# Optimization experiments

Hardware: AMD Instinct MI355X
Metric: run time of the kernel (lower is better)

The kernel has to match this reference:

```python
import jax, jax.numpy as jnp
import numpy as np

N_HEAD = 12

def setup_inputs() -> dict:
    key = jax.random.key(0)
    ks = jax.random.split(key, 5)
    B, T, C = 4, 2048, 768
    scale = 0.02
    return {
        "x": jax.random.normal(ks[0], (B, T, C), dtype=jnp.float32),
        "W_attn": jax.random.normal(ks[1], (C, 3 * C), dtype=jnp.float32) * scale,
        "b_attn": jax.random.normal(ks[2], (3 * C,), dtype=jnp.float32) * scale,
        "W_proj": jax.random.normal(ks[3], (C, C), dtype=jnp.float32) * scale,
        "b_proj": jax.random.normal(ks[4], (C,), dtype=jnp.float32) * scale,
    }

def reference(x, W_attn, b_attn, W_proj, b_proj):
    B, T, C = x.shape
    H = N_HEAD
    D = C // H  # head dim
    qkv = x @ W_attn + b_attn  # [B,T,3C]
    q, k, v = jnp.split(qkv, 3, axis=-1)
    # [B,H,T,D]
    q = q.reshape(B, T, H, D).transpose(0, 2, 1, 3)
    k = k.reshape(B, T, H, D).transpose(0, 2, 1, 3)
    v = v.reshape(B, T, H, D).transpose(0, 2, 1, 3)
    scores = jnp.einsum('bhqd,bhkd->bhqk', q, k) / jnp.sqrt(jnp.float32(D))
    causal = jnp.tril(jnp.ones((T, T), dtype=bool))
    scores = jnp.where(causal[None, None, :, :], scores, jnp.float32(-jnp.inf))
    attn = jax.nn.softmax(scores, axis=-1)
    out = jnp.einsum('bhqk,bhkd->bhqd', attn, v)  # [B,H,T,D]
    out = out.transpose(0, 2, 1, 3).reshape(B, T, C)
    return out @ W_proj + b_proj
```

## Files before the change

kernel.cpp:

```cpp
#include <hip/hip_runtime.h>

typedef float f32x4 __attribute__((ext_vector_type(4)));
typedef __bf16 bf16x8 __attribute__((ext_vector_type(8)));
typedef unsigned short u16x8 __attribute__((ext_vector_type(8)));
typedef unsigned short u16x4 __attribute__((ext_vector_type(4)));

#define MFMA16(a, b, c) __builtin_amdgcn_mfma_f32_16x16x32_bf16((a), (b), (c), 0, 0, 0)

__device__ __forceinline__ unsigned short f2bf(float f) {
    __bf16 h = (__bf16)f;
    union { __bf16 h; unsigned short u; } c; c.h = h;
    return c.u;
}

__device__ __forceinline__ void gload_lds16(const unsigned short* g, unsigned short* l) {
    __builtin_amdgcn_global_load_lds(
        (const __attribute__((address_space(1))) unsigned int*)g,
        (__attribute__((address_space(3))) unsigned int*)l, 16, 0, 0);
}

__global__ void k_convert_bf16(const float* __restrict__ in,
                               unsigned short* __restrict__ out, int n) {
    int i = (blockIdx.x * 256 + threadIdx.x) * 4;
    if (i + 3 < n) {
        float4 v = *reinterpret_cast<const float4*>(in + i);
        ushort4 o;
        o.x = f2bf(v.x); o.y = f2bf(v.y); o.z = f2bf(v.z); o.w = f2bf(v.w);
        *reinterpret_cast<ushort4*>(out + i) = o;
    }
}

__global__ void k_transpose_bf16(const float* __restrict__ in,
                                 unsigned short* __restrict__ out, int R, int C) {
    __shared__ unsigned short tile[32][33];
    int bx = blockIdx.x * 32;
    int by = blockIdx.y * 32;
    int tx = threadIdx.x;
    int ty = threadIdx.y;
    #pragma unroll
    for (int i = ty; i < 32; i += 8)
        tile[i][tx] = f2bf(in[(size_t)(by + i) * C + bx + tx]);
    __syncthreads();
    #pragma unroll
    for (int i = ty; i < 32; i += 8)
        out[(size_t)(bx + i) * R + by + tx] = tile[tx][i];
}

template<int EPI>
__global__ __launch_bounds__(512) void k_gemm_bt(
    const unsigned short* __restrict__ A,
    const unsigned short* __restrict__ Bt,
    const float* __restrict__ bias,
    unsigned short* __restrict__ Qo,
    unsigned short* __restrict__ Ko,
    unsigned short* __restrict__ Vto,
    float* __restrict__ Co,
    int K)
{
    __shared__ unsigned short SM[(256 + 128) * 64];
    unsigned short* As = SM;
    unsigned short* Bs = SM + 256 * 64;
    const int nwg = gridDim.x * gridDim.y;
    const int bid0 = blockIdx.y * gridDim.x + blockIdx.x;
    const int logical = (bid0 & 7) * (nwg >> 3) + (bid0 >> 3);
    const int bm = logical / gridDim.x;
    const int bn = logical % gridDim.x;
    const int tid = threadIdx.x;
    const int w = tid >> 6, l = tid & 63;
    const int wm = w >> 1, wn = w & 1;
    const int ln = l & 15, kb = l >> 4;

    f32x4 acc[4][4];
    #pragma unroll
    for (int i = 0; i < 4; ++i)
        #pragma unroll
        for (int j = 0; j < 4; ++j)
            #pragma unroll
            for (int r = 0; r < 4; ++r) acc[i][j][r] = 0.f;

    const unsigned short* Ab = A + (size_t)(bm * 256) * K;
    const unsigned short* Bb = Bt + (size_t)(bn * 128) * K;

    const int srow = tid >> 3;
    const int sslot = tid & 7;
    const int csw = (sslot ^ (srow & 7)) * 8;

    for (int k0 = 0; k0 < K; k0 += 64) {
        #pragma unroll
        for (int j = 0; j < 4; ++j) {
            const int r = j * 64 + srow;
            gload_lds16(&Ab[(size_t)r * K + k0 + csw], &As[r * 64 + sslot * 8]);
        }
        #pragma unroll
        for (int j = 0; j < 2; ++j) {
            const int r = j * 64 + srow;
            gload_lds16(&Bb[(size_t)r * K + k0 + csw], &Bs[r * 64 + sslot * 8]);
        }
        __syncthreads();
        #pragma unroll
        for (int kh = 0; kh < 2; ++kh) {
            bf16x8 af[4], bfr[4];
            #pragma unroll
            for (int mt = 0; mt < 4; ++mt) {
                const int row = wm * 64 + mt * 16 + ln;
                const int slot = ((kh << 2) | kb) ^ (row & 7);
                af[mt] = *reinterpret_cast<const bf16x8*>(&As[row * 64 + slot * 8]);
            }
            #pragma unroll
            for (int nt = 0; nt < 4; ++nt) {
                const int row = wn * 64 + nt * 16 + ln;
                const int slot = ((kh << 2) | kb) ^ (row & 7);
                bfr[nt] = *reinterpret_cast<const bf16x8*>(&Bs[row * 64 + slot * 8]);
            }
            #pragma unroll
            for (int mt = 0; mt < 4; ++mt)
                #pragma unroll
                for (int nt = 0; nt < 4; ++nt)
                    acc[mt][nt] = MFMA16(af[mt], bfr[nt], acc[mt][nt]);
        }
        __syncthreads();
    }

    const float SC = 0.1803368801111204f;

    if (EPI == 0 && bn >= 12) {
        unsigned short* Ts = SM;
        const int cl_w = wn * 64;
        #pragma unroll
        for (int hh2 = 0; hh2 < 2; ++hh2) {
            if ((wm >> 1) == hh2) {
                #pragma unroll
                for (int mt = 0; mt < 4; ++mt) {
                    #pragma unroll
                    for (int nt = 0; nt < 4; ++nt) {
                        const int cl = cl_w + nt * 16 + ln;
                        const float bv = bias[bn * 128 + cl];
                        #pragma unroll
                        for (int r = 0; r < 4; ++r) {
                            const int rl = (wm & 1) * 64 + mt * 16 + kb * 4 + r;
                            const int pos = cl * 128 + ((((rl >> 3) ^ (cl & 7)) << 3) | (rl & 7));
                            Ts[pos] = f2bf(acc[mt][nt][r] + bv);
                        }
                    }
                }
            }
            __syncthreads();
            {
                const int cl = tid >> 2;
                const int col = bn * 128 + cl;
                const int cc = col - 1536;
                const int hh = cc >> 6, dd = cc & 63;
                #pragma unroll
                for (int j8 = 0; j8 < 4; ++j8) {
                    const int rb = (tid & 3) * 4 + j8;
                    u16x8 val = *reinterpret_cast<const u16x8*>(&Ts[cl * 128 + ((rb ^ (cl & 7)) << 3)]);
                    const int tg = bm * 256 + hh2 * 128 + rb * 8;
                    const int bb = tg >> 11;
                    const int tloc = tg & 2047;
                    const int grp = tloc & ~31;
                    const int jj = (tloc >> 3) & 3;
                    const int tlo = grp + 8 * ((2 * jj) & 3) + 4 * (jj >> 1);
                    const int thi = grp + 8 * ((2 * jj + 1) & 3) + 4 * (jj >> 1);
                    unsigned short* basep = &Vto[((size_t)((bb * 12 + hh) * 64 + dd)) * 2048];
                    *reinterpret_cast<u16x4*>(basep + tlo) =
                        __builtin_shufflevector(val, val, 0, 1, 2, 3);
                    *reinterpret_cast<u16x4*>(basep + thi) =
                        __builtin_shufflevector(val, val, 4, 5, 6, 7);
                }
            }
            __syncthreads();
        }
        return;
    }

    #pragma unroll
    for (int mt = 0; mt < 4; ++mt) {
        #pragma unroll
        for (int nt = 0; nt < 4; ++nt) {
            const int col = bn * 128 + wn * 64 + nt * 16 + ln;
            #pragma unroll
            for (int r = 0; r < 4; ++r) {
                const int row = bm * 256 + wm * 64 + mt * 16 + kb * 4 + r;
                float v = acc[mt][nt][r] + bias[col];
                if (EPI == 0) {
                    int cc = col >= 768 ? col - 768 : col;
                    int h = cc >> 6, d = cc & 63;
                    int b = row >> 11, t = row & 2047;
                    if (col < 768)
                        Qo[((size_t)((b * 12 + h) * 2048 + t)) * 64 + d] = f2bf(v * SC);
                    else
                        Ko[((size_t)((b * 12 + h) * 2048 + t)) * 64 + d] = f2bf(v);
                } else {
                    Co[(size_t)row * 768 + col] = v;
                }
            }
        }
    }
}

__global__ __launch_bounds__(256) void k_attn(
    const unsigned short* __restrict__ Q,
    const unsigned short* __restrict__ Kk,
    const unsigned short* __restrict__ Vt,
    unsigned short* __restrict__ Oo)
{
    __shared__ unsigned short Ks[2][64 * 64];
    __shared__ unsigned short Vs[2][64 * 64];
    const int bid0 = blockIdx.x;
    const int xcd = bid0 & 7;
    const int loc = bid0 >> 3;
    const int qb = 15 - (loc / 6);
    const int bh = xcd * 6 + (loc % 6);
    const int tid = threadIdx.x;
    const int w = tid >> 6, l = tid & 63;
    const int ln = l & 15, kb = l >> 4;
    const int kbq = kb * 4;
    const int b = bh / 12, h = bh - b * 12;
    const int q0w = qb * 128 + w * 32;

    const unsigned short* Qb = Q + (size_t)bh * 2048 * 64;
    const unsigned short* Kb = Kk + (size_t)bh * 2048 * 64;
    const unsigned short* Vb = Vt + (size_t)bh * 64 * 2048;

    bf16x8 qf[2][2];
    #pragma unroll
    for (int qn = 0; qn < 2; ++qn) {
        const unsigned short* qr = &Qb[(size_t)(q0w + qn * 16 + ln) * 64 + kb * 8];
        qf[qn][0] = *reinterpret_cast<const bf16x8*>(qr);
        qf[qn][1] = *reinterpret_cast<const bf16x8*>(qr + 32);
    }

    bf16x8 vones;
    #pragma unroll
    for (int e = 0; e < 8; ++e) vones[e] = (__bf16)1.0f;
    const f32x4 fzero = {0.f, 0.f, 0.f, 0.f};

    f32x4 oaccT[2][4];
    f32x4 den[2];
    #pragma unroll
    for (int qn = 0; qn < 2; ++qn) {
        #pragma unroll
        for (int r = 0; r < 4; ++r) den[qn][r] = 0.f;
        #pragma unroll
        for (int dt = 0; dt < 4; ++dt)
            #pragma unroll
            for (int r = 0; r < 4; ++r) oaccT[qn][dt][r] = 0.f;
    }

    const int srow = tid >> 3;
    const int sslot = tid & 7;
    const int csw = (sslot ^ (srow & 7)) * 8;
    const int ntile = 2 * qb + 2;
    const int lastkt = (q0w + 31) >> 6;

    #define STAGE(kt_, buf_)                                                        \
        {                                                                           \
            const int kb_ = (kt_) * 64;                                             \
            _Pragma("unroll")                                                       \
            for (int j = 0; j < 2; ++j) {                                           \
                const int r = j * 32 + srow;                                        \
                gload_lds16(&Kb[(size_t)(kb_ + r) * 64 + csw],                      \
                            &Ks[buf_][r * 64 + sslot * 8]);                         \
                gload_lds16(&Vb[(size_t)r * 2048 + kb_ + csw],                      \
                            &Vs[buf_][r * 64 + sslot * 8]);                         \
            }                                                                       \
        }

    STAGE(0, 0);

    for (int kt = 0; kt < ntile; ++kt) {
        const int buf = kt & 1;
        asm volatile("s_waitcnt vmcnt(0)" ::: "memory");
        __builtin_amdgcn_sched_barrier(0);
        __builtin_amdgcn_s_barrier();
        if (kt + 1 < ntile) STAGE(kt + 1, buf ^ 1);

        if (kt <= lastkt) {
            const int kbase = kt * 64;
            const unsigned short* Ksb = &Ks[buf][0];
            const unsigned short* Vsb = &Vs[buf][0];
            bf16x8 kf[4][2];
            #pragma unroll
            for (int km = 0; km < 4; ++km) {
                const int row = km * 16 + ln;
                #pragma unroll
                for (int dh = 0; dh < 2; ++dh) {
                    const int slot = ((dh << 2) | kb) ^ (row & 7);
                    kf[km][dh] = *reinterpret_cast<const bf16x8*>(&Ksb[row * 64 + slot * 8]);
                }
            }
            f32x4 st[4][2];
            __builtin_amdgcn_s_setprio(1);
            #pragma unroll
            for (int km = 0; km < 4; ++km)
                #pragma unroll
                for (int qn = 0; qn < 2; ++qn) {
                    st[km][qn] = MFMA16(kf[km][0], qf[qn][0], fzero);
                    st[km][qn] = MFMA16(kf[km][1], qf[qn][1], st[km][qn]);
                }
            __builtin_amdgcn_s_setprio(0);
            bf16x8 vf[4][2];
            #pragma unroll
            for (int dt = 0; dt < 4; ++dt) {
                const int row = dt * 16 + ln;
                #pragma unroll
                for (int kh = 0; kh < 2; ++kh) {
                    const int slot = ((kh << 2) | kb) ^ (row & 7);
                    vf[dt][kh] = *reinterpret_cast<const bf16x8*>(&Vsb[row * 64 + slot * 8]);
                }
            }

            const bool diag = (kt == lastkt);
            #pragma unroll
            for (int qn = 0; qn < 2; ++qn) {
                const int qrow = q0w + qn * 16 + ln;
                #pragma unroll
                for (int km = 0; km < 4; ++km) {
                    #pragma unroll
                    for (int r = 0; r < 4; ++r) {
                        float sv = st[km][qn][r];
                        if (diag) {
                            const int key = kbase + km * 16 + kbq + r;
                            sv = (key <= qrow) ? sv : -1e30f;
                        }
                        st[km][qn][r] = __builtin_amdgcn_exp2f(sv);
                    }
                }
            }
            bf16x8 pa[2][2];
            #pragma unroll
            for (int qn = 0; qn < 2; ++qn)
                #pragma unroll
                for (int kh = 0; kh < 2; ++kh) {
                    bf16x8 t;
                    #pragma unroll
                    for (int r = 0; r < 4; ++r) {
                        t[r]     = (__bf16)st[2 * kh][qn][r];
                        t[r + 4] = (__bf16)st[2 * kh + 1][qn][r];
                    }
                    pa[qn][kh] = t;
                }
            __builtin_amdgcn_s_setprio(1);
            #pragma unroll
            for (int qn = 0; qn < 2; ++qn) {
                #pragma unroll
                for (int dt = 0; dt < 4; ++dt) {
                    oaccT[qn][dt] = MFMA16(pa[qn][0], vf[dt][0], oaccT[qn][dt]);
                    oaccT[qn][dt] = MFMA16(pa[qn][1], vf[dt][1], oaccT[qn][dt]);
                }
                den[qn] = MFMA16(pa[qn][0], vones, den[qn]);
                den[qn] = MFMA16(pa[qn][1], vones, den[qn]);
            }
            __builtin_amdgcn_s_setprio(0);
        }
    }

    #pragma unroll
    for (int qn = 0; qn < 2; ++qn) {
        #pragma unroll
        for (int r = 0; r < 4; ++r) {
            const float inv = 1.0f / den[qn][r];
            const int t = q0w + qn * 16 + kbq + r;
            #pragma unroll
            for (int dt = 0; dt < 4; ++dt)
                Oo[((size_t)(b * 2048 + t)) * 768 + h * 64 + dt * 16 + ln] =
                    f2bf(oaccT[qn][dt][r] * inv);
        }
    }
}

extern "C" void kernel_launch(void* const* d_in, const int* in_sizes, int n_in,
                              void* d_out, int out_size, void* d_ws, size_t ws_size,
                              hipStream_t stream) {
    const float* x      = (const float*)d_in[0];
    const float* W_attn = (const float*)d_in[1];
    const float* b_attn = (const float*)d_in[2];
    const float* W_proj = (const float*)d_in[3];
    const float* b_proj = (const float*)d_in[4];
    float* out = (float*)d_out;

    char* ws = (char*)d_ws;
    const size_t SZ_X  = (size_t)8192 * 768 * 2;
    const size_t SZ_WA = (size_t)2304 * 768 * 2;
    const size_t SZ_WP = (size_t)768 * 768 * 2;
    const size_t SZ_T  = (size_t)8192 * 768 * 2;

    unsigned short* x_bf = (unsigned short*)(ws);
    unsigned short* wa_t = (unsigned short*)(ws + SZ_X);
    unsigned short* wp_t = (unsigned short*)(ws + SZ_X + SZ_WA);
    unsigned short* Qb   = (unsigned short*)(ws + SZ_X + SZ_WA + SZ_WP);
    unsigned short* Kb   = (unsigned short*)(ws + SZ_X + SZ_WA + SZ_WP + SZ_T);
    unsigned short* Vtb  = (unsigned short*)(ws + SZ_X + SZ_WA + SZ_WP + 2 * SZ_T);
    unsigned short* attn_o = x_bf;

    k_convert_bf16<<<6144, 256, 0, stream>>>(x, x_bf, 8192 * 768);
    dim3 tb(32, 8);
    k_transpose_bf16<<<dim3(2304 / 32, 768 / 32), tb, 0, stream>>>(W_attn, wa_t, 768, 2304);
    k_transpose_bf16<<<dim3(768 / 32, 768 / 32), tb, 0, stream>>>(W_proj, wp_t, 768, 768);
    k_gemm_bt<0><<<dim3(18, 32), 512, 0, stream>>>(x_bf, wa_t, b_attn, Qb, Kb, Vtb, nullptr, 768);
    k_attn<<<768, 256, 0, stream>>>(Qb, Kb, Vtb, attn_o);
    k_gemm_bt<1><<<dim3(6, 32), 512, 0, stream>>>(attn_o, wp_t, b_proj, nullptr, nullptr, nullptr, out, 768);
}
```

Measured before the change: 138.8 us.

## Make attention single-wave blocks loading K/V directly into registers

```diff
diff --git a/kernel.cpp b/kernel.cpp
--- a/kernel.cpp
+++ b/kernel.cpp
@@ -198,25 +198,23 @@
     }
 }
 
-__global__ __launch_bounds__(256) void k_attn(
+__global__ __launch_bounds__(64) void k_attn(
     const unsigned short* __restrict__ Q,
     const unsigned short* __restrict__ Kk,
     const unsigned short* __restrict__ Vt,
     unsigned short* __restrict__ Oo)
 {
-    __shared__ unsigned short Ks[2][64 * 64];
-    __shared__ unsigned short Vs[2][64 * 64];
     const int bid0 = blockIdx.x;
     const int xcd = bid0 & 7;
-    const int loc = bid0 >> 3;
-    const int qb = 15 - (loc / 6);
-    const int bh = xcd * 6 + (loc % 6);
+    const int idx = bid0 >> 3;
+    const int hloc = idx % 6;
+    const int qc = 63 - idx / 6;
+    const int bh = xcd * 6 + hloc;
     const int tid = threadIdx.x;
-    const int w = tid >> 6, l = tid & 63;
-    const int ln = l & 15, kb = l >> 4;
+    const int ln = tid & 15, kb = tid >> 4;
     const int kbq = kb * 4;
     const int b = bh / 12, h = bh - b * 12;
-    const int q0w = qb * 128 + w * 32;
+    const int q0w = qc * 32;
 
     const unsigned short* Qb = Q + (size_t)bh * 2048 * 64;
     const unsigned short* Kb = Kk + (size_t)bh * 2048 * 64;
@@ -247,111 +245,91 @@
             for (int r = 0; r < 4; ++r) oaccT[qn][dt][r] = 0.f;
     }
 
-    const int srow = tid >> 3;
-    const int sslot = tid & 7;
-    const int csw = (sslot ^ (srow & 7)) * 8;
-    const int ntile = 2 * qb + 2;
-    const int lastkt = (q0w + 31) >> 6;
-
-    #define STAGE(kt_, buf_)                                                        \
-        {                                                                           \
-            const int kb_ = (kt_) * 64;                                             \
-            _Pragma("unroll")                                                       \
-            for (int j = 0; j < 2; ++j) {                                           \
-                const int r = j * 32 + srow;                                        \
-                gload_lds16(&Kb[(size_t)(kb_ + r) * 64 + csw],                      \
-                            &Ks[buf_][r * 64 + sslot * 8]);                         \
-                gload_lds16(&Vb[(size_t)r * 2048 + kb_ + csw],                      \
-                            &Vs[buf_][r * 64 + sslot * 8]);                         \
-            }                                                                       \
-        }
-
-    STAGE(0, 0);
+    const int ntile = (q0w + 31) / 64 + 1;
+    const int lastkt = ntile - 1;
+
+    bf16x8 kf[4][2], vf[4][2];
+    #pragma unroll
+    for (int km = 0; km < 4; ++km) {
+        const unsigned short* kr = &Kb[(size_t)(km * 16 + ln) * 64 + kb * 8];
+        kf[km][0] = *reinterpret_cast<const bf16x8*>(kr);
+        kf[km][1] = *reinterpret_cast<const bf16x8*>(kr + 32);
+    }
+    #pragma unroll
+    for (int dt = 0; dt < 4; ++dt) {
+        const unsigned short* vr = &Vb[(size_t)(dt * 16 + ln) * 2048 + kb * 8];
+        vf[dt][0] = *reinterpret_cast<const bf16x8*>(vr);
+        vf[dt][1] = *reinterpret_cast<const bf16x8*>(vr + 32);
+    }
 
     for (int kt = 0; kt < ntile; ++kt) {
-        const int buf = kt & 1;
-        asm volatile("s_waitcnt vmcnt(0)" ::: "memory");
-        __builtin_amdgcn_sched_barrier(0);
-        __builtin_amdgcn_s_barrier();
-        if (kt + 1 < ntile) STAGE(kt + 1, buf ^ 1);
-
-        if (kt <= lastkt) {
-            const int kbase = kt * 64;
-            const unsigned short* Ksb = &Ks[buf][0];
-            const unsigned short* Vsb = &Vs[buf][0];
-            bf16x8 kf[4][2];
+        const int kbase = kt * 64;
+        f32x4 st[4][2];
+        #pragma unroll
+        for (int km = 0; km < 4; ++km)
+            #pragma unroll
+            for (int qn = 0; qn < 2; ++qn) {
+                st[km][qn] = MFMA16(kf[km][0], qf[qn][0], fzero);
+                st[km][qn] = MFMA16(kf[km][1], qf[qn][1], st[km][qn]);
+            }
+        if (kt + 1 < ntile) {
+            const int nb = kbase + 64;
             #pragma unroll
             for (int km = 0; km < 4; ++km) {
-                const int row = km * 16 + ln;
-                #pragma unroll
-                for (int dh = 0; dh < 2; ++dh) {
-                    const int slot = ((dh << 2) | kb) ^ (row & 7);
-                    kf[km][dh] = *reinterpret_cast<const bf16x8*>(&Ksb[row * 64 + slot * 8]);
-                }
-            }
-            f32x4 st[4][2];
-            __builtin_amdgcn_s_setprio(1);
-            #pragma unroll
-            for (int km = 0; km < 4; ++km)
-                #pragma unroll
-                for (int qn = 0; qn < 2; ++qn) {
-                    st[km][qn] = MFMA16(kf[km][0], qf[qn][0], fzero);
-                    st[km][qn] = MFMA16(kf[km][1], qf[qn][1], st[km][qn]);
-                }
-            __builtin_amdgcn_s_setprio(0);
-            bf16x8 vf[4][2];
+                const unsigned short* kr = &Kb[(size_t)(nb + km * 16 + ln) * 64 + kb * 8];
+                kf[km][0] = *reinterpret_cast<const bf16x8*>(kr);
+                kf[km][1] = *reinterpret_cast<const bf16x8*>(kr + 32);
+            }
+        }
+
+        const bool diag = (kt == lastkt);
+        #pragma unroll
+        for (int qn = 0; qn < 2; ++qn) {
+            const int qrow = q0w + qn * 16 + ln;
+            #pragma unroll
+            for (int km = 0; km < 4; ++km) {
+                #pragma unroll
+                for (int r = 0; r < 4; ++r) {
+                    float sv = st[km][qn][r];
+                    if (diag) {
+                        const int key = kbase + km * 16 + kbq + r;
+                        sv = (key <= qrow) ? sv : -1e30f;
+                    }
+                    st[km][qn][r] = __builtin_amdgcn_exp2f(sv);
+                }
+            }
+        }
+        bf16x8 pa[2][2];
+        #pragma unroll
+        for (int qn = 0; qn < 2; ++qn)
+            #pragma unroll
+            for (int kh = 0; kh < 2; ++kh) {
+                bf16x8 t;
+                #pragma unroll
+                for (int r = 0; r < 4; ++r) {
+                    t[r]     = (__bf16)st[2 * kh][qn][r];
+                    t[r + 4] = (__bf16)st[2 * kh + 1][qn][r];
+                }
+                pa[qn][kh] = t;
+            }
+        #pragma unroll
+        for (int qn = 0; qn < 2; ++qn) {
             #pragma unroll
             for (int dt = 0; dt < 4; ++dt) {
-                const int row = dt * 16 + ln;
-                #pragma unroll
-                for (int kh = 0; kh < 2; ++kh) {
-                    const int slot = ((kh << 2) | kb) ^ (row & 7);
-                    vf[dt][kh] = *reinterpret_cast<const bf16x8*>(&Vsb[row * 64 + slot * 8]);
-                }
-            }
-
-            const bool diag = (kt == lastkt);
-            #pragma unroll
-            for (int qn = 0; qn < 2; ++qn) {
-                const int qrow = q0w + qn * 16 + ln;
-                #pragma unroll
-                for (int km = 0; km < 4; ++km) {
-                    #pragma unroll
-                    for (int r = 0; r < 4; ++r) {
-                        float sv = st[km][qn][r];
-                        if (diag) {
-                            const int key = kbase + km * 16 + kbq + r;
-                            sv = (key <= qrow) ? sv : -1e30f;
-                        }
-                        st[km][qn][r] = __builtin_amdgcn_exp2f(sv);
-                    }
-                }
-            }
-            bf16x8 pa[2][2];
-            #pragma unroll
-            for (int qn = 0; qn < 2; ++qn)
-                #pragma unroll
-                for (int kh = 0; kh < 2; ++kh) {
-                    bf16x8 t;
-                    #pragma unroll
-                    for (int r = 0; r < 4; ++r) {
-                        t[r]     = (__bf16)st[2 * kh][qn][r];
-                        t[r + 4] = (__bf16)st[2 * kh + 1][qn][r];
-                    }
-                    pa[qn][kh] = t;
-                }
-            __builtin_amdgcn_s_setprio(1);
-            #pragma unroll
-            for (int qn = 0; qn < 2; ++qn) {
-                #pragma unroll
-                for (int dt = 0; dt < 4; ++dt) {
-                    oaccT[qn][dt] = MFMA16(pa[qn][0], vf[dt][0], oaccT[qn][dt]);
-                    oaccT[qn][dt] = MFMA16(pa[qn][1], vf[dt][1], oaccT[qn][dt]);
-                }
-                den[qn] = MFMA16(pa[qn][0], vones, den[qn]);
-                den[qn] = MFMA16(pa[qn][1], vones, den[qn]);
-            }
-            __builtin_amdgcn_s_setprio(0);
+                oaccT[qn][dt] = MFMA16(pa[qn][0], vf[dt][0], oaccT[qn][dt]);
+                oaccT[qn][dt] = MFMA16(pa[qn][1], vf[dt][1], oaccT[qn][dt]);
+            }
+            den[qn] = MFMA16(pa[qn][0], vones, den[qn]);
+            den[qn] = MFMA16(pa[qn][1], vones, den[qn]);
+        }
+        if (kt + 1 < ntile) {
+            const int nb = kbase + 64;
+            #pragma unroll
+            for (int dt = 0; dt < 4; ++dt) {
+                const unsigned short* vr = &Vb[(size_t)(dt * 16 + ln) * 2048 + nb + kb * 8];
+                vf[dt][0] = *reinterpret_cast<const bf16x8*>(vr);
+                vf[dt][1] = *reinterpret_cast<const bf16x8*>(vr + 32);
+            }
         }
     }
 
@@ -398,6 +376,6 @@
     k_transpose_bf16<<<dim3(2304 / 32, 768 / 32), tb, 0, stream>>>(W_attn, wa_t, 768, 2304);
     k_transpose_bf16<<<dim3(768 / 32, 768 / 32), tb, 0, stream>>>(W_proj, wp_t, 768, 768);
     k_gemm_bt<0><<<dim3(18, 32), 512, 0, stream>>>(x_bf, wa_t, b_attn, Qb, Kb, Vtb, nullptr, 768);
-    k_attn<<<768, 256, 0, stream>>>(Qb, Kb, Vtb, attn_o);
+    k_attn<<<3072, 64, 0, stream>>>(Qb, Kb, Vtb, attn_o);
     k_gemm_bt<1><<<dim3(6, 32), 512, 0, stream>>>(attn_o, wp_t, b_proj, nullptr, nullptr, nullptr, out, 768);
 }
```

Result: slower. 178.6 us (+28.7%).
